# Kernel tuning notes

Measured on AMD Instinct MI355X. Metric: run time of the kernel, lower is better.

## Reference

```python
import jax, jax.numpy as jnp
import numpy as np

B, S, D, H = 1, 2048, 2048, 32
HD = D // H  # head_dim = 64
FF = 4 * D
EPS = 1e-5


def _alibi_slopes(n_heads):
    # standard ALiBi slopes for power-of-2 head counts: 2^(-8i/n)
    return np.array([2.0 ** (-8.0 * (i + 1) / n_heads) for i in range(n_heads)], np.float32)


def setup_inputs() -> dict:
    key = jax.random.key(0)
    ks = jax.random.split(key, 16)
    s = 0.02
    x = jax.random.normal(ks[0], (B, S, D), jnp.float32)
    # alibi bias [B, H, 1, S], broadcast over query positions (HF views alibi as (b, h, 1, kv_len))
    slopes = _alibi_slopes(H)
    alibi_np = slopes[:, None, None] * np.arange(S, dtype=np.float32)[None, None, :]
    alibi = jnp.broadcast_to(jnp.asarray(alibi_np), (B, H, 1, S))
    # additive causal mask [1, 1, S, S]
    causal = np.tril(np.ones((S, S), bool))
    attention_mask = jnp.asarray(np.where(causal, 0.0, -1e9).astype(np.float32))[None, None]
    p = lambda k, shp: s * jax.random.normal(k, shp, jnp.float32)
    return {
        "x": x,
        "alibi": alibi,
        "attention_mask": attention_mask,
        "ln1_g": jnp.ones((D,), jnp.float32), "ln1_b": jnp.zeros((D,), jnp.float32),
        "ln2_g": jnp.ones((D,), jnp.float32), "ln2_b": jnp.zeros((D,), jnp.float32),
        "wqkv": p(ks[1], (D, 3 * D)), "bqkv": jnp.zeros((3 * D,), jnp.float32),
        "wo": p(ks[2], (D, D)), "bo": jnp.zeros((D,), jnp.float32),
        "w1": p(ks[3], (D, FF)), "b1": jnp.zeros((FF,), jnp.float32),
        "w2": p(ks[4], (FF, D)), "b2": jnp.zeros((D,), jnp.float32),
    }


def _layernorm(h, g, b):
    m = h.mean(-1, keepdims=True)
    v = ((h - m) ** 2).mean(-1, keepdims=True)
    return (h - m) * jax.lax.rsqrt(v + EPS) * g + b


def reference(x, alibi, attention_mask, ln1_g, ln1_b, ln2_g, ln2_b,
              wqkv, bqkv, wo, bo, w1, b1, w2, b2):
    b, s, d = x.shape
    inv_norm = 1.0 / np.sqrt(HD).astype(np.float32)
    # --- input layernorm ---
    h = _layernorm(x, ln1_g, ln1_b)
    # --- fused QKV ---
    qkv = h @ wqkv + bqkv
    q, k, v = jnp.split(qkv, 3, axis=-1)
    q = q.reshape(b, s, H, HD).transpose(0, 2, 1, 3)  # [b, h, s, hd]
    k = k.reshape(b, s, H, HD).transpose(0, 2, 1, 3)
    v = v.reshape(b, s, H, HD).transpose(0, 2, 1, 3)
    # --- ALiBi-biased attention (HF falcon alibi path) ---
    scores = jnp.einsum("bhqd,bhkd->bhqk", q, k)          # [b, h, s, s]
    logits = (scores + alibi) * inv_norm + attention_mask  # alibi broadcasts over q dim
    probs = jax.nn.softmax(logits, axis=-1)
    ctx = jnp.einsum("bhqk,bhkd->bhqd", probs, v)
    ctx = ctx.transpose(0, 2, 1, 3).reshape(b, s, d)
    attn_out = ctx @ wo + bo
    # --- residual, post-attn layernorm, MLP (non-parallel falcon-rw layout) ---
    res = x + attn_out
    h2 = _layernorm(res, ln2_g, ln2_b)
    mlp = jax.nn.gelu(h2 @ w1 + b1, approximate=False) @ w2 + b2
    return res + mlp
```

## Files before the change

### kernel.cpp

```cpp
#include <hip/hip_runtime.h>
#include <hip/hip_bf16.h>
#include <cstdint>
#include <cstddef>

static constexpr int Sq  = 2048;
static constexpr int Dm  = 2048;
static constexpr int NH  = 32;
static constexpr int HDm = 64;
static constexpr int FFm = 8192;

typedef __bf16 bf16x8 __attribute__((ext_vector_type(8)));
typedef float  f32x4  __attribute__((ext_vector_type(4)));

__device__ __forceinline__ void async_ld16(const void* g, void* l) {
  __builtin_amdgcn_global_load_lds((const __attribute__((address_space(1))) void*)g,
                                   (__attribute__((address_space(3))) void*)l, 16, 0, 0);
}

__global__ __launch_bounds__(256)
void tcast_kernel(const float* __restrict__ in, __hip_bfloat16* __restrict__ out,
                  int K, int N) {
  __shared__ float tile[64][65];
  const int tc = blockIdx.x * 64;
  const int tr = blockIdx.y * 64;
  const int cx = threadIdx.x & 63;
  const int ry = threadIdx.x >> 6;
#pragma unroll
  for (int i = 0; i < 16; ++i) {
    int r = ry + i * 4;
    tile[r][cx] = in[(size_t)(tr + r) * N + tc + cx];
  }
  __syncthreads();
#pragma unroll
  for (int i = 0; i < 16; ++i) {
    int r = ry + i * 4;
    out[(size_t)(tc + r) * K + tr + cx] = __float2bfloat16(tile[cx][r]);
  }
}

__global__ __launch_bounds__(256)
void ln_kernel(const float* __restrict__ x, const float* __restrict__ g,
               const float* __restrict__ b, __hip_bfloat16* __restrict__ out) {
  __shared__ float red[4];
  const int t = threadIdx.x;
  const float* xr = x + (size_t)blockIdx.x * Dm;
  float v[8];
  float s = 0.f;
#pragma unroll
  for (int i = 0; i < 8; ++i) { v[i] = xr[t + i * 256]; s += v[i]; }
#pragma unroll
  for (int off = 32; off > 0; off >>= 1) s += __shfl_down(s, off, 64);
  if ((t & 63) == 0) red[t >> 6] = s;
  __syncthreads();
  const float mean = (red[0] + red[1] + red[2] + red[3]) * (1.f / Dm);
  __syncthreads();
  float vs = 0.f;
#pragma unroll
  for (int i = 0; i < 8; ++i) { float d = v[i] - mean; vs += d * d; }
#pragma unroll
  for (int off = 32; off > 0; off >>= 1) vs += __shfl_down(vs, off, 64);
  if ((t & 63) == 0) red[t >> 6] = vs;
  __syncthreads();
  const float inv = rsqrtf((red[0] + red[1] + red[2] + red[3]) * (1.f / Dm) + 1e-5f);
  __hip_bfloat16* orow = out + (size_t)blockIdx.x * Dm;
#pragma unroll
  for (int i = 0; i < 8; ++i) {
    int c = t + i * 256;
    orow[c] = __float2bfloat16((v[i] - mean) * inv * g[c] + b[c]);
  }
}

template <int EPI>
__global__ __launch_bounds__(256)
void gemm_kernel(const __hip_bfloat16* __restrict__ A,
                 const __hip_bfloat16* __restrict__ Bt,
                 int N, int K, int Ksub,
                 const float* __restrict__ bias,
                 const float* __restrict__ addsrc,
                 float* __restrict__ outf,
                 __hip_bfloat16* __restrict__ outb,
                 __hip_bfloat16* __restrict__ qo,
                 __hip_bfloat16* __restrict__ ko,
                 __hip_bfloat16* __restrict__ vo,
                 __hip_bfloat16* __restrict__ po) {
  __shared__ __align__(16) __hip_bfloat16 As[2][128 * 32];
  __shared__ __align__(16) __hip_bfloat16 Bs[2][128 * 32];
  const int t = threadIdx.x;
  const int lane = t & 63, w = t >> 6, quad = lane >> 4, l16 = lane & 15;
  const int nbx = gridDim.x;
  const int id = blockIdx.y * nbx + blockIdx.x;
  const int chunk = (nbx * 16) >> 3;
  const int nid = (id & 7) * chunk + (id >> 3);
  const int bn = nid >> 4, bm = nid & 15;
  const int bz = blockIdx.z;
  const int wm = (w & 1) * 64, wn = (w >> 1) * 64;
  const __hip_bfloat16* Abase = A + (size_t)bm * 128 * K;
  const __hip_bfloat16* Bbase = Bt + (size_t)bn * 128 * K;
  const int kBeg = bz * Ksub;
  const int kSteps = Ksub / 32;

  const int c0 = t, c1 = t + 256;
  const int r0 = c0 >> 2, g0 = ((c0 & 3) - (r0 >> 1)) & 3;
  const int r1 = c1 >> 2, g1 = ((c1 & 3) - (r1 >> 1)) & 3;
  const __hip_bfloat16* a0p = Abase + (size_t)r0 * K + g0 * 8;
  const __hip_bfloat16* a1p = Abase + (size_t)r1 * K + g1 * 8;
  const __hip_bfloat16* b0p = Bbase + (size_t)r0 * K + g0 * 8;
  const __hip_bfloat16* b1p = Bbase + (size_t)r1 * K + g1 * 8;

  struct Stage { bf16x8 a0, a1, b0, b1; };
  auto gload = [&](int k0) {
    Stage s;
    s.a0 = *(const bf16x8*)(a0p + k0);
    s.a1 = *(const bf16x8*)(a1p + k0);
    s.b0 = *(const bf16x8*)(b0p + k0);
    s.b1 = *(const bf16x8*)(b1p + k0);
    return s;
  };
  auto swrite = [&](int b, const Stage& s) {
    *(bf16x8*)(&As[b][c0 * 8]) = s.a0;
    *(bf16x8*)(&As[b][c1 * 8]) = s.a1;
    *(bf16x8*)(&Bs[b][c0 * 8]) = s.b0;
    *(bf16x8*)(&Bs[b][c1 * 8]) = s.b1;
  };

  f32x4 acc[4][4] = {};
  auto compute = [&](int b) {
    bf16x8 af[4], bfv[4];
#pragma unroll
    for (int i = 0; i < 4; ++i) {
      int row = wm + i * 16 + l16;
      int p = (quad + (row >> 1)) & 3;
      af[i] = *(const bf16x8*)(&As[b][row * 32 + p * 8]);
    }
#pragma unroll
    for (int i = 0; i < 4; ++i) {
      int row = wn + i * 16 + l16;
      int p = (quad + (row >> 1)) & 3;
      bfv[i] = *(const bf16x8*)(&Bs[b][row * 32 + p * 8]);
    }
#pragma unroll
    for (int mt = 0; mt < 4; ++mt)
#pragma unroll
      for (int nt = 0; nt < 4; ++nt)
        acc[mt][nt] = __builtin_amdgcn_mfma_f32_16x16x32_bf16(af[mt], bfv[nt], acc[mt][nt], 0, 0, 0);
  };

#define BAR() asm volatile("s_waitcnt lgkmcnt(0)\ns_barrier" ::: "memory")
  Stage s0 = gload(kBeg);
  Stage s1 = gload(kBeg + 32);
  swrite(0, s0);
  BAR();
  for (int i = 0; i < kSteps; i += 2) {
    if (i + 2 < kSteps) s0 = gload(kBeg + (i + 2) * 32);
    compute(0);
    swrite(1, s1);
    BAR();
    if (i + 3 < kSteps) s1 = gload(kBeg + (i + 3) * 32);
    compute(1);
    if (i + 2 < kSteps) swrite(0, s0);
    BAR();
  }
#undef BAR

#pragma unroll
  for (int mt = 0; mt < 4; ++mt) {
#pragma unroll
    for (int nt = 0; nt < 4; ++nt) {
      const int n = bn * 128 + wn + nt * 16 + l16;
      const float bz2 = bias[n];
#pragma unroll
      for (int r = 0; r < 4; ++r) {
        const int m = bm * 128 + wm + mt * 16 + quad * 4 + r;
        float val = acc[mt][nt][r];
        if constexpr (EPI == 0) {
          val += bz2;
          int which = n >> 11, d2 = n & 2047;
          int hh = d2 >> 6, hd = d2 & 63;
          if (which == 0)
            qo[((size_t)hh * Sq + m) * HDm + hd] = __float2bfloat16(val * 0.125f);
          else if (which == 1)
            ko[((size_t)hh * Sq + m) * HDm + hd] = __float2bfloat16(val);
          else
            vo[((size_t)hh * HDm + hd) * Sq + m] = __float2bfloat16(val);
        } else if constexpr (EPI == 1) {
          outf[(size_t)m * N + n] = addsrc[(size_t)m * N + n] + bz2 + val;
        } else if constexpr (EPI == 2) {
          val += bz2;
          float gg = 0.5f * val * (1.0f + erff(val * 0.70710678118654752f));
          outb[(size_t)m * N + n] = __float2bfloat16(gg);
        } else {
          if (bz == 0)
            outf[(size_t)m * N + n] = addsrc[(size_t)m * N + n] + bz2 + val;
          else
            po[(size_t)m * N + n] = __float2bfloat16(val);
        }
      }
    }
  }
}

__global__ __launch_bounds__(256)
void addp_kernel(float* __restrict__ out, const __hip_bfloat16* __restrict__ p) {
  const int i = (blockIdx.x * 256 + threadIdx.x) * 4;
  float4 o = *(const float4*)(out + i);
  const __hip_bfloat16* pp = p + i;
  o.x += (float)pp[0]; o.y += (float)pp[1]; o.z += (float)pp[2]; o.w += (float)pp[3];
  *(float4*)(out + i) = o;
}

__global__ __launch_bounds__(256)
void attn_kernel(const __hip_bfloat16* __restrict__ qb,
                 const __hip_bfloat16* __restrict__ kb,
                 const __hip_bfloat16* __restrict__ vt,
                 const float* __restrict__ alibi,
                 __hip_bfloat16* __restrict__ ctx) {
  __shared__ __align__(16) __hip_bfloat16 Kl[2][64 * 64];
  __shared__ __align__(16) __hip_bfloat16 Vl[2][64 * 64];
  __shared__ __align__(16) __hip_bfloat16 Pl[4][16 * 64];
  const int pi = blockIdx.x, h = blockIdx.y;
  const int qA = pi, qB = (Sq / 64 - 1) - pi;
  const int t = threadIdx.x, w = t >> 6, lane = t & 63, quad = lane >> 4, l16 = lane & 15;
  const __hip_bfloat16* qh = qb + (size_t)h * Sq * HDm;
  const __hip_bfloat16* kh = kb + (size_t)h * Sq * HDm;
  const __hip_bfloat16* vh = vt + (size_t)h * HDm * Sq;
  const float* al = alibi + (size_t)h * Sq;

  const int rA = qA * 64 + w * 16 + l16;
  const int rB = qB * 64 + w * 16 + l16;
  const bf16x8 qA0 = *(const bf16x8*)(qh + (size_t)rA * HDm + quad * 8);
  const bf16x8 qA1 = *(const bf16x8*)(qh + (size_t)rA * HDm + 32 + quad * 8);
  const bf16x8 qB0 = *(const bf16x8*)(qh + (size_t)rB * HDm + quad * 8);
  const bf16x8 qB1 = *(const bf16x8*)(qh + (size_t)rB * HDm + 32 + quad * 8);

  auto stageS = [&](int b, int s) {
    const int kbk = (s <= qA) ? s : s - qA - 1;
#pragma unroll
    for (int j = 0; j < 2; ++j) {
      int c = j * 256 + t;
      int row = c >> 3;
      int swz = (c & 7) ^ (row & 7);
      async_ld16(kh + (size_t)(kbk * 64 + row) * HDm + swz * 8, &Kl[b][c * 8]);
      async_ld16(vh + (size_t)row * Sq + kbk * 64 + swz * 8, &Vl[b][c * 8]);
    }
  };

  f32x4 o[4] = {};
  float m_i[4], l_i[4];
#pragma unroll
  for (int r = 0; r < 4; ++r) { m_i[r] = -3e38f; l_i[r] = 0.f; }

  const int total = qA + qB + 2;
  stageS(0, 0);
  int buf = 0;
  for (int s = 0; s < total; ++s, buf ^= 1) {
    __syncthreads();
    if (s + 1 < total) stageS(buf ^ 1, s + 1);
    const bool ph = (s > qA);
    const int kbk = ph ? s - qA - 1 : s;
    const int qblk = ph ? qB : qA;
    const bf16x8 a0 = ph ? qB0 : qA0;
    const bf16x8 a1 = ph ? qB1 : qA1;

    f32x4 sf[4];
    const f32x4 zero = {};
#pragma unroll
    for (int nt = 0; nt < 4; ++nt) {
      int row = nt * 16 + l16;
      bf16x8 kf0 = *(const bf16x8*)(&Kl[buf][row * 64 + ((quad ^ (row & 7)) << 3)]);
      bf16x8 kf1 = *(const bf16x8*)(&Kl[buf][row * 64 + (((4 + quad) ^ (row & 7)) << 3)]);
      sf[nt] = __builtin_amdgcn_mfma_f32_16x16x32_bf16(a0, kf0, zero, 0, 0, 0);
      sf[nt] = __builtin_amdgcn_mfma_f32_16x16x32_bf16(a1, kf1, sf[nt], 0, 0, 0);
    }
    const bool diag = (kbk == qblk);
    float mrow[4] = {-3e38f, -3e38f, -3e38f, -3e38f};
#pragma unroll
    for (int nt = 0; nt < 4; ++nt) {
      const float ab = al[kbk * 64 + nt * 16 + l16] * 0.125f;
      const int kcol = nt * 16 + l16;
#pragma unroll
      for (int r = 0; r < 4; ++r) {
        float vv = sf[nt][r] + ab;
        if (diag && kcol > w * 16 + quad * 4 + r) vv = -3e38f;
        sf[nt][r] = vv;
        mrow[r] = fmaxf(mrow[r], vv);
      }
    }
#pragma unroll
    for (int off = 8; off > 0; off >>= 1)
#pragma unroll
      for (int r = 0; r < 4; ++r)
        mrow[r] = fmaxf(mrow[r], __shfl_xor(mrow[r], off, 64));
    float alpha[4], rs[4], p[4][4];
#pragma unroll
    for (int r = 0; r < 4; ++r) {
      float mn = fmaxf(m_i[r], mrow[r]);
      alpha[r] = __expf(m_i[r] - mn);
      m_i[r] = mn;
    }
#pragma unroll
    for (int nt = 0; nt < 4; ++nt)
#pragma unroll
      for (int r = 0; r < 4; ++r) p[nt][r] = __expf(sf[nt][r] - m_i[r]);
#pragma unroll
    for (int r = 0; r < 4; ++r) rs[r] = p[0][r] + p[1][r] + p[2][r] + p[3][r];
#pragma unroll
    for (int off = 8; off > 0; off >>= 1)
#pragma unroll
      for (int r = 0; r < 4; ++r) rs[r] += __shfl_xor(rs[r], off, 64);
#pragma unroll
    for (int r = 0; r < 4; ++r) l_i[r] = l_i[r] * alpha[r] + rs[r];
#pragma unroll
    for (int dt = 0; dt < 4; ++dt)
#pragma unroll
      for (int r = 0; r < 4; ++r) o[dt][r] *= alpha[r];
    __hip_bfloat16* pw = &Pl[w][0];
#pragma unroll
    for (int nt = 0; nt < 4; ++nt)
#pragma unroll
      for (int r = 0; r < 4; ++r) {
        int prow = quad * 4 + r;
        int e = nt * 16 + l16;
        int c16 = e >> 3;
        pw[prow * 64 + ((c16 ^ (prow & 7)) << 3) + (e & 7)] = __float2bfloat16(p[nt][r]);
      }
    asm volatile("s_waitcnt lgkmcnt(0)" ::: "memory");
    const bf16x8 pa0 = *(const bf16x8*)(pw + l16 * 64 + ((quad ^ (l16 & 7)) << 3));
    const bf16x8 pa1 = *(const bf16x8*)(pw + l16 * 64 + (((4 + quad) ^ (l16 & 7)) << 3));
#pragma unroll
    for (int dt = 0; dt < 4; ++dt) {
      int row = dt * 16 + l16;
      bf16x8 v0 = *(const bf16x8*)(&Vl[buf][row * 64 + ((quad ^ (row & 7)) << 3)]);
      bf16x8 v1 = *(const bf16x8*)(&Vl[buf][row * 64 + (((4 + quad) ^ (row & 7)) << 3)]);
      o[dt] = __builtin_amdgcn_mfma_f32_16x16x32_bf16(pa0, v0, o[dt], 0, 0, 0);
      o[dt] = __builtin_amdgcn_mfma_f32_16x16x32_bf16(pa1, v1, o[dt], 0, 0, 0);
    }
    if (s == qA) {
#pragma unroll
      for (int dt = 0; dt < 4; ++dt)
#pragma unroll
        for (int r = 0; r < 4; ++r) {
          int srow = qA * 64 + w * 16 + quad * 4 + r;
          ctx[(size_t)srow * Dm + h * HDm + dt * 16 + l16] =
              __float2bfloat16(o[dt][r] / l_i[r]);
          o[dt][r] = 0.f;
        }
#pragma unroll
      for (int r = 0; r < 4; ++r) { m_i[r] = -3e38f; l_i[r] = 0.f; }
    }
  }
#pragma unroll
  for (int dt = 0; dt < 4; ++dt)
#pragma unroll
    for (int r = 0; r < 4; ++r) {
      int srow = qB * 64 + w * 16 + quad * 4 + r;
      ctx[(size_t)srow * Dm + h * HDm + dt * 16 + l16] =
          __float2bfloat16(o[dt][r] / l_i[r]);
    }
}

extern "C" void kernel_launch(void* const* d_in, const int* in_sizes, int n_in,
                              void* d_out, int out_size, void* d_ws, size_t ws_size,
                              hipStream_t stream) {
  const float* x     = (const float*)d_in[0];
  const float* alibi = (const float*)d_in[1];
  const float* ln1g  = (const float*)d_in[3];
  const float* ln1b  = (const float*)d_in[4];
  const float* ln2g  = (const float*)d_in[5];
  const float* ln2b  = (const float*)d_in[6];
  const float* wqkv  = (const float*)d_in[7];
  const float* bqkv  = (const float*)d_in[8];
  const float* wo    = (const float*)d_in[9];
  const float* bo    = (const float*)d_in[10];
  const float* w1    = (const float*)d_in[11];
  const float* b1    = (const float*)d_in[12];
  const float* w2    = (const float*)d_in[13];
  const float* b2    = (const float*)d_in[14];
  float* out = (float*)d_out;

  char* p = (char*)d_ws;
  auto alloc = [&](size_t bytes) {
    char* r = p;
    p += (bytes + 255) & ~(size_t)255;
    return r;
  };
  constexpr size_t SD2 = (size_t)Sq * Dm * 2;
  char* R2 = alloc((size_t)FFm * Dm * 2);
  char* R1 = alloc(4 * SD2);
  __hip_bfloat16* hb   = (__hip_bfloat16*)alloc(SD2);
  float*          resb = (float*)alloc((size_t)Sq * Dm * 4);

  __hip_bfloat16* wqkvT = (__hip_bfloat16*)R2;
  __hip_bfloat16* w1T   = (__hip_bfloat16*)R2;
  __hip_bfloat16* w2T   = (__hip_bfloat16*)R2;
  __hip_bfloat16* qbuf  = (__hip_bfloat16*)(R1 + 0 * SD2);
  __hip_bfloat16* kbuf  = (__hip_bfloat16*)(R1 + 1 * SD2);
  __hip_bfloat16* vtbuf = (__hip_bfloat16*)(R1 + 2 * SD2);
  __hip_bfloat16* ctxb  = (__hip_bfloat16*)(R1 + 3 * SD2);
  __hip_bfloat16* woT   = (__hip_bfloat16*)(R1 + 0 * SD2);
  __hip_bfloat16* t1b   = (__hip_bfloat16*)R1;
  __hip_bfloat16* part  = hb;

  tcast_kernel<<<dim3(3 * Dm / 64, Dm / 64), 256, 0, stream>>>(wqkv, wqkvT, Dm, 3 * Dm);
  ln_kernel<<<Sq, 256, 0, stream>>>(x, ln1g, ln1b, hb);
  gemm_kernel<0><<<dim3(3 * Dm / 128, Sq / 128), 256, 0, stream>>>(
      hb, wqkvT, 3 * Dm, Dm, Dm, bqkv, nullptr, nullptr, nullptr, qbuf, kbuf, vtbuf, nullptr);
  tcast_kernel<<<dim3(FFm / 64, Dm / 64), 256, 0, stream>>>(w1, w1T, Dm, FFm);
  attn_kernel<<<dim3(Sq / 128, NH), 256, 0, stream>>>(qbuf, kbuf, vtbuf, alibi, ctxb);
  tcast_kernel<<<dim3(Dm / 64, Dm / 64), 256, 0, stream>>>(wo, woT, Dm, Dm);
  gemm_kernel<3><<<dim3(Dm / 128, Sq / 128, 2), 256, 0, stream>>>(
      ctxb, woT, Dm, Dm, Dm / 2, bo, x, resb, nullptr, nullptr, nullptr, nullptr, part);
  addp_kernel<<<(Sq * Dm) / 1024, 256, 0, stream>>>(resb, part);
  ln_kernel<<<Sq, 256, 0, stream>>>(resb, ln2g, ln2b, hb);
  gemm_kernel<2><<<dim3(FFm / 128, Sq / 128), 256, 0, stream>>>(
      hb, w1T, FFm, Dm, Dm, b1, nullptr, nullptr, t1b, nullptr, nullptr, nullptr, nullptr);
  tcast_kernel<<<dim3(Dm / 64, FFm / 64), 256, 0, stream>>>(w2, w2T, FFm, Dm);
  gemm_kernel<3><<<dim3(Dm / 128, Sq / 128, 2), 256, 0, stream>>>(
      t1b, w2T, Dm, FFm, FFm / 2, b2, resb, out, nullptr, nullptr, nullptr, nullptr, part);
  addp_kernel<<<(Sq * Dm) / 1024, 256, 0, stream>>>(out, part);
}
```

Before: 665.5 us.

## Use async global-to-LDS loads for GEMM double buffering

Replaces the register-staged global loads and LDS writes in the GEMM main loop with direct global_load_lds async copies into the alternate buffer. The loop becomes a single-step double buffer that waits on vmcnt before each barrier. This removes the VGPR staging and the explicit ds_write instructions, which may lower register pressure. In exchange the prefetch distance is one step instead of two, and each barrier now waits on global memory latency.

After: 667.2 us. Within noise of the previous version (+0.3%).

```diff
diff --git a/kernel.cpp b/kernel.cpp
--- a/kernel.cpp
+++ b/kernel.cpp
@@ -107,20 +107,11 @@
   const __hip_bfloat16* b0p = Bbase + (size_t)r0 * K + g0 * 8;
   const __hip_bfloat16* b1p = Bbase + (size_t)r1 * K + g1 * 8;
 
-  struct Stage { bf16x8 a0, a1, b0, b1; };
-  auto gload = [&](int k0) {
-    Stage s;
-    s.a0 = *(const bf16x8*)(a0p + k0);
-    s.a1 = *(const bf16x8*)(a1p + k0);
-    s.b0 = *(const bf16x8*)(b0p + k0);
-    s.b1 = *(const bf16x8*)(b1p + k0);
-    return s;
-  };
-  auto swrite = [&](int b, const Stage& s) {
-    *(bf16x8*)(&As[b][c0 * 8]) = s.a0;
-    *(bf16x8*)(&As[b][c1 * 8]) = s.a1;
-    *(bf16x8*)(&Bs[b][c0 * 8]) = s.b0;
-    *(bf16x8*)(&Bs[b][c1 * 8]) = s.b1;
+  auto stage = [&](int b, int k0) {
+    async_ld16(a0p + k0, &As[b][c0 * 8]);
+    async_ld16(a1p + k0, &As[b][c1 * 8]);
+    async_ld16(b0p + k0, &Bs[b][c0 * 8]);
+    async_ld16(b1p + k0, &Bs[b][c1 * 8]);
   };
 
   f32x4 acc[4][4] = {};
@@ -145,22 +136,17 @@
         acc[mt][nt] = __builtin_amdgcn_mfma_f32_16x16x32_bf16(af[mt], bfv[nt], acc[mt][nt], 0, 0, 0);
   };
 
-#define BAR() asm volatile("s_waitcnt lgkmcnt(0)\ns_barrier" ::: "memory")
-  Stage s0 = gload(kBeg);
-  Stage s1 = gload(kBeg + 32);
-  swrite(0, s0);
-  BAR();
-  for (int i = 0; i < kSteps; i += 2) {
-    if (i + 2 < kSteps) s0 = gload(kBeg + (i + 2) * 32);
-    compute(0);
-    swrite(1, s1);
-    BAR();
-    if (i + 3 < kSteps) s1 = gload(kBeg + (i + 3) * 32);
-    compute(1);
-    if (i + 2 < kSteps) swrite(0, s0);
-    BAR();
-  }
-#undef BAR
+#define PIPE_BAR() asm volatile("s_waitcnt vmcnt(0)\n\ts_barrier" ::: "memory")
+  stage(0, kBeg);
+  PIPE_BAR();
+  int buf = 0;
+  for (int i = 0; i < kSteps; ++i) {
+    if (i + 1 < kSteps) stage(buf ^ 1, kBeg + (i + 1) * 32);
+    compute(buf);
+    PIPE_BAR();
+    buf ^= 1;
+  }
+#undef PIPE_BAR
 
 #pragma unroll
   for (int mt = 0; mt < 4; ++mt) {
```
